# Kernel tuning notes

Measured on AMD Instinct MI355X. Metric: run time of the kernel, lower is better.

## Reference

```python
import jax, jax.numpy as jnp
import numpy as np

D_EMBED, D_K, D_V = 1024, 64, 64
B, S = 4, 4096


def setup_inputs() -> dict:
    key = jax.random.key(0)
    k1, k2, k3, k4 = jax.random.split(key, 4)
    x = jax.random.normal(k1, (B, S, D_EMBED), dtype=jnp.float32)
    # nn.Linear(d_embed, d) stores weight as [d, d_embed]
    Wq = jax.random.normal(k2, (D_K, D_EMBED), dtype=jnp.float32) * (D_EMBED ** -0.5)
    Wk = jax.random.normal(k3, (D_K, D_EMBED), dtype=jnp.float32) * (D_EMBED ** -0.5)
    Wv = jax.random.normal(k4, (D_V, D_EMBED), dtype=jnp.float32) * (D_EMBED ** -0.5)
    return {"x": x, "Wq": Wq, "Wk": Wk, "Wv": Wv}


def reference(x, Wq, Wk, Wv):
    # self-attention: y = z = x
    key = jnp.einsum('bse,ke->bsk', x, Wk)
    query = jnp.einsum('bse,ke->bsk', x, Wq)
    value = jnp.einsum('bse,ve->bsv', x, Wv)
    d_k = key.shape[-1]
    weight = jnp.einsum('bqk,bsk->bqs', query, key) / (d_k ** 0.5)
    # Faithful to torch: tril then masked_fill(weight == 0, -inf)
    weight = jnp.tril(weight)
    weight = jnp.where(weight == 0, -jnp.inf, weight)
    weight = jax.nn.softmax(weight, axis=-1)
    return jnp.einsum('bqs,bsv->bqv', weight, value)
```

## Files before the change

### kernel.cpp

```cpp
#include <hip/hip_runtime.h>
#include <hip/hip_bf16.h>


typedef short s16x8 __attribute__((ext_vector_type(8)));
typedef float f32x4 __attribute__((ext_vector_type(4)));
typedef float f32x16 __attribute__((ext_vector_type(16)));
typedef unsigned u32x2 __attribute__((ext_vector_type(2)));

#define MFMA16(a, b, c) __builtin_amdgcn_mfma_f32_16x16x32_bf16(a, b, c, 0, 0, 0)
#define MFMA32(a, b, c) __builtin_amdgcn_mfma_f32_32x32x16_bf16(a, b, c, 0, 0, 0)

constexpr int SEQ = 4096;
constexpr int DE  = 1024;

__device__ __forceinline__ short f2bf(float f) {
    union { float f; unsigned u; } v; v.f = f;
    unsigned r = (v.u + 0x7FFFu + ((v.u >> 16) & 1u)) >> 16;
    return (short)r;
}
__device__ __forceinline__ unsigned fbits(float f) { union { float f; unsigned u; } v; v.f = f; return v.u; }
__device__ __forceinline__ float bitsf(unsigned u) { union { unsigned u; float f; } v; v.u = u; return v.f; }
__device__ __forceinline__ unsigned pk2(float a, float b) {
    return (fbits(b) & 0xFFFF0000u) | (fbits(a) >> 16);
}

#define GLDS(gp, lp)                                                          \
    __builtin_amdgcn_global_load_lds(                                         \
        (const __attribute__((address_space(1))) unsigned int*)(gp),          \
        (__attribute__((address_space(3))) unsigned int*)(lp), 16, 0, 0)

__global__ __launch_bounds__(256) void k_convw(const float* __restrict__ Wq,
                                               const float* __restrict__ Wk,
                                               const float* __restrict__ Wv,
                                               short* __restrict__ Wb) {
    int i = (blockIdx.x * 256 + threadIdx.x) * 4;
    if (i >= 192 * 1024) return;
    int n = i >> 10, k = i & 1023;
    const float* src; float sc;
    if (n < 64)       { src = Wq + n * 1024;         sc = 0.18033688011112042f; }
    else if (n < 128) { src = Wk + (n - 64) * 1024;  sc = 1.0f; }
    else              { src = Wv + (n - 128) * 1024; sc = 1.0f; }
    float4 v = *(const float4*)(src + k);
    short4 o;
    o.x = f2bf(v.x * sc); o.y = f2bf(v.y * sc);
    o.z = f2bf(v.z * sc); o.w = f2bf(v.w * sc);
    *(short4*)(Wb + i) = o;
}

__global__ __launch_bounds__(512) void k_proj(const float* __restrict__ x,
                                              const short* __restrict__ Wb,
                                              short* __restrict__ Qs,
                                              short* __restrict__ Ks,
                                              short* __restrict__ Vt) {
    __shared__ __align__(16) char lds[2][40960];
    const int tid  = threadIdx.x;
    const int lane = tid & 63;
    const int c = lane & 15, g = (lane >> 4) & 3;
    const int wv = tid >> 6;
    const int rg = wv & 3, nh = wv >> 2;
    const int n0 = nh * 96;
    const int m0 = blockIdx.x * 64;

    const int Ar  = tid >> 4;
    const int Acs = ((tid & 15) << 4) ^ ((Ar & 7) << 4);
    const char* aS0 = (const char*)x + (((size_t)(m0 + Ar)) << 12) + Acs;
    const char* aS1 = aS0 + ((size_t)32 << 12);
    const int Wr  = tid >> 3;
    const int Wcs = ((tid & 7) << 4) ^ ((Wr & 7) << 4);
    const char* wS0 = (const char*)Wb + (((size_t)Wr) << 11) + Wcs;
    const char* wS1 = wS0 + ((size_t)64 << 11);
    const char* wS2 = wS0 + ((size_t)128 << 11);

    char* db0 = &lds[0][0] + tid * 16;
    char* db1 = &lds[1][0] + tid * 16;

    const int arow = rg * 16 + c;
    const int swz  = (c & 7) << 4;
    const char* aR[2] = { &lds[0][0] + arow * 256, &lds[1][0] + arow * 256 };
    const char* wR[2][6];
#pragma unroll
    for (int nf = 0; nf < 6; nf++) {
        int wrow = n0 + nf * 16 + c;
        wR[0][nf] = &lds[0][0] + 16384 + wrow * 128;
        wR[1][nf] = &lds[1][0] + 16384 + wrow * 128;
    }

    f32x4 acc[6];
#pragma unroll
    for (int i = 0; i < 6; i++) acc[i] = (f32x4){0.f, 0.f, 0.f, 0.f};

#define PSTAGE(kk, db) {                                  \
        GLDS(aS0 + (kk) * 256, (db));                     \
        GLDS(aS1 + (kk) * 256, (db) + 8192);              \
        GLDS(wS0 + (kk) * 128, (db) + 16384);             \
        GLDS(wS1 + (kk) * 128, (db) + 24576);             \
        GLDS(wS2 + (kk) * 128, (db) + 32768); }

#define PCOMPUTE(bi) {                                                         \
        _Pragma("unroll")                                                      \
        for (int kc = 0; kc < 2; kc++) {                                       \
            float4 a0 = *(const float4*)(aR[bi] + ((kc*128 + g*32)      ^ swz)); \
            float4 a1 = *(const float4*)(aR[bi] + ((kc*128 + g*32 + 16) ^ swz)); \
            s16x8 a;                                                           \
            a[0]=f2bf(a0.x); a[1]=f2bf(a0.y); a[2]=f2bf(a0.z); a[3]=f2bf(a0.w); \
            a[4]=f2bf(a1.x); a[5]=f2bf(a1.y); a[6]=f2bf(a1.z); a[7]=f2bf(a1.w); \
            _Pragma("unroll")                                                  \
            for (int nf = 0; nf < 6; nf++) {                                   \
                s16x8 bfr = *(const s16x8*)(wR[bi][nf] + ((kc*64 + g*16) ^ swz)); \
                acc[nf] = MFMA16(a, bfr, acc[nf]);                             \
            }                                                                  \
        } }

    PSTAGE(0, db0);
    PSTAGE(1, db1);

    for (int kk = 0; kk < 15; kk++) {
        asm volatile("s_waitcnt vmcnt(5)" ::: "memory");
        __builtin_amdgcn_sched_barrier(0);
        __builtin_amdgcn_s_barrier();
        if (kk & 1) PCOMPUTE(1) else PCOMPUTE(0)
        asm volatile("s_waitcnt lgkmcnt(0)" ::: "memory");
        __builtin_amdgcn_sched_barrier(0);
        __builtin_amdgcn_s_barrier();
        if (kk < 14) { if (kk & 1) PSTAGE(kk + 2, db1) else PSTAGE(kk + 2, db0) }
    }
    asm volatile("s_waitcnt vmcnt(0)" ::: "memory");
    __builtin_amdgcn_sched_barrier(0);
    __builtin_amdgcn_s_barrier();
    PCOMPUTE(1)
#undef PSTAGE
#undef PCOMPUTE

#pragma unroll
    for (int nf = 0; nf < 6; nf++) {
        int col16 = n0 + nf * 16;
        if (col16 < 64) {
            int col = col16 + c;
#pragma unroll
            for (int r = 0; r < 4; r++)
                Qs[(size_t)(m0 + rg * 16 + g * 4 + r) * 64 + col] = f2bf(acc[nf][r]);
        } else if (col16 < 128) {
            int col = col16 - 64 + c;
#pragma unroll
            for (int r = 0; r < 4; r++)
                Ks[(size_t)(m0 + rg * 16 + g * 4 + r) * 64 + col] = f2bf(acc[nf][r]);
        } else {
            int d  = col16 - 128 + c;
            int mm = m0 + rg * 16 + g * 4;
            int bt = mm >> 12, s0 = mm & (SEQ - 1);
            short4 o;
            o.x = f2bf(acc[nf][0]); o.y = f2bf(acc[nf][1]);
            o.z = f2bf(acc[nf][2]); o.w = f2bf(acc[nf][3]);
            *(short4*)(Vt + ((size_t)(bt * 64 + d)) * SEQ + s0) = o;
        }
    }
}

__global__ __launch_bounds__(256) void k_attn(const short* __restrict__ Qs,
                                              const short* __restrict__ Ks,
                                              const short* __restrict__ Vt,
                                              float* __restrict__ out) {
    __shared__ __align__(16) char smem[65536];
    float (*pO)[64][33] = (float (*)[64][33])smem;
    float* pM = (float*)(smem + 33792);
    float* pL = pM + 128;

    int tid = threadIdx.x;
    int l = tid & 63, wv = tid >> 6;
    int q = l & 31, hi = l >> 5;
    int bid = blockIdx.x;
    int j = 127 - (bid >> 2), bt = bid & 3;
    int q0 = j * 32;
    const int kend = q0 + 32;
    const int R = (kend + 127) >> 7;

    const short* Qb = Qs + (size_t)bt * SEQ * 64;
    const short* Kb = Ks + (size_t)bt * SEQ * 64;
    const short* Vb = Vt + (size_t)bt * 64 * SEQ;

    s16x8 qf[4];
#pragma unroll
    for (int d = 0; d < 4; d++)
        qf[d] = *(const s16x8*)(Qb + (size_t)(q0 + q) * 64 + d * 16 + hi * 8);

    const int kr  = l >> 3;
    const int kch = (l & 7) ^ kr;
    const int vr  = l >> 4;

#define ASTAGE(kbase, bufb) {                                                  \
        _Pragma("unroll")                                                      \
        for (int i = 0; i < 4; i++)                                            \
            GLDS(Kb + (((size_t)((kbase) + wv*32 + i*8 + kr)) << 6) + kch*8,   \
                 smem + (bufb)*32768 + (wv*4 + i)*1024);                       \
        _Pragma("unroll")                                                      \
        for (int i = 0; i < 4; i++)                                            \
            GLDS(Vb + (size_t)(wv*16 + i*4 + vr) * SEQ + (kbase)               \
                    + (((l & 15) ^ (i*4 + vr)) * 8),                           \
                 smem + (bufb)*32768 + 16384 + (wv*4 + i)*1024); }

    f32x16 o0 = {}, o1 = {};
    float m = -1e30f, ll = 0.f;

    ASTAGE(0, 0);
    ASTAGE(128, 1);

    for (int r = 0; r < R; r++) {
        if (r == R - 1) asm volatile("s_waitcnt vmcnt(0)" ::: "memory");
        else            asm volatile("s_waitcnt vmcnt(8)" ::: "memory");
        __builtin_amdgcn_sched_barrier(0);
        __builtin_amdgcn_s_barrier();
        __builtin_amdgcn_sched_barrier(0);

        int k0 = r * 128 + wv * 32;
        if (k0 < kend) {
            const char* kb = smem + (r & 1) * 32768 + (wv * 32 + q) * 128;
            int ks = q & 7;
            s16x8 ka0 = *(const s16x8*)(kb + (((hi    ) ^ ks) << 4));
            s16x8 ka1 = *(const s16x8*)(kb + (((hi + 2) ^ ks) << 4));
            s16x8 ka2 = *(const s16x8*)(kb + (((hi + 4) ^ ks) << 4));
            s16x8 ka3 = *(const s16x8*)(kb + (((hi + 6) ^ ks) << 4));
            f32x16 s = {};
            s = MFMA32(ka0, qf[0], s);
            s = MFMA32(ka1, qf[1], s);
            s = MFMA32(ka2, qf[2], s);
            s = MFMA32(ka3, qf[3], s);

            if (k0 + 31 > q0) {
#pragma unroll
                for (int rr = 0; rr < 16; rr++) {
                    int kk = k0 + (rr & 3) + 8 * (rr >> 2) + 4 * hi;
                    if (kk > q0 + q) s[rr] = -3.0e38f;
                }
            }

            float t0 = fmaxf(fmaxf(fmaxf(s[0], s[1]), fmaxf(s[2], s[3])),
                             fmaxf(fmaxf(s[4], s[5]), fmaxf(s[6], s[7])));
            float t1 = fmaxf(fmaxf(fmaxf(s[8], s[9]), fmaxf(s[10], s[11])),
                             fmaxf(fmaxf(s[12], s[13]), fmaxf(s[14], s[15])));
            float tm = fmaxf(t0, t1);
            u32x2 sw = __builtin_amdgcn_permlane32_swap(fbits(tm), fbits(tm), false, false);
            tm = fmaxf(bitsf(sw[0]), bitsf(sw[1]));
            float mn = fmaxf(m, tm);
            float scale = __builtin_amdgcn_exp2f(m - mn);
            m = mn;
#pragma unroll
            for (int rr = 0; rr < 16; rr++) s[rr] = __builtin_amdgcn_exp2f(s[rr] - mn);
            float u0s = ((s[0] + s[1]) + (s[2] + s[3])) + ((s[4] + s[5]) + (s[6] + s[7]));
            float u1s = ((s[8] + s[9]) + (s[10] + s[11])) + ((s[12] + s[13]) + (s[14] + s[15]));
            float ts = u0s + u1s;
            sw = __builtin_amdgcn_permlane32_swap(fbits(ts), fbits(ts), false, false);
            ts = bitsf(sw[0]) + bitsf(sw[1]);
            ll = ll * scale + ts;
            o0 *= scale; o1 *= scale;

            unsigned A0 = pk2(s[0], s[1]),   B0 = pk2(s[2], s[3]);
            unsigned A1 = pk2(s[4], s[5]),   B1 = pk2(s[6], s[7]);
            unsigned A2 = pk2(s[8], s[9]),   B2 = pk2(s[10], s[11]);
            unsigned A3 = pk2(s[12], s[13]), B3 = pk2(s[14], s[15]);
            u32x2 r0 = __builtin_amdgcn_permlane32_swap(A0, A1, false, false);
            u32x2 r1 = __builtin_amdgcn_permlane32_swap(B0, B1, false, false);
            u32x2 r2 = __builtin_amdgcn_permlane32_swap(A2, A3, false, false);
            u32x2 r3 = __builtin_amdgcn_permlane32_swap(B2, B3, false, false);
            union { unsigned u[4]; s16x8 v; } p0u, p1u;
            p0u.u[0] = r0[0]; p0u.u[1] = r1[0]; p0u.u[2] = r0[1]; p0u.u[3] = r1[1];
            p1u.u[0] = r2[0]; p1u.u[1] = r3[0]; p1u.u[2] = r2[1]; p1u.u[3] = r3[1];

            const char* vbb = smem + (r & 1) * 32768 + 16384;
            int vc0 = ((4 * wv + hi)     ^ (q & 15)) << 4;
            int vc1 = ((4 * wv + hi + 2) ^ (q & 15)) << 4;
            const char* v0p = vbb + q * 256;
            const char* v1p = vbb + (q + 32) * 256;
            o0 = MFMA32(*(const s16x8*)(v0p + vc0), p0u.v, o0);
            o0 = MFMA32(*(const s16x8*)(v0p + vc1), p1u.v, o0);
            o1 = MFMA32(*(const s16x8*)(v1p + vc0), p0u.v, o1);
            o1 = MFMA32(*(const s16x8*)(v1p + vc1), p1u.v, o1);
        }

        asm volatile("s_waitcnt lgkmcnt(0)" ::: "memory");
        __builtin_amdgcn_sched_barrier(0);
        __builtin_amdgcn_s_barrier();
        if (r + 2 < R) { if (r & 1) ASTAGE((r + 2) * 128, 1) else ASTAGE((r + 2) * 128, 0) }
    }
#undef ASTAGE

#pragma unroll
    for (int rr = 0; rr < 16; rr++) {
        int dv = (rr & 3) + 8 * (rr >> 2) + 4 * hi;
        pO[wv][dv][q]      = o0[rr];
        pO[wv][dv + 32][q] = o1[rr];
    }
    if (hi == 0) { pM[wv * 32 + q] = m; pL[wv * 32 + q] = ll; }
    __syncthreads();

    int q2 = tid >> 3, d0 = (tid & 7) * 8;
    float m0v = pM[q2], m1v = pM[32 + q2], m2v = pM[64 + q2], m3v = pM[96 + q2];
    float M = fmaxf(fmaxf(m0v, m1v), fmaxf(m2v, m3v));
    float w0 = __builtin_amdgcn_exp2f(m0v - M);
    float w1 = __builtin_amdgcn_exp2f(m1v - M);
    float w2 = __builtin_amdgcn_exp2f(m2v - M);
    float w3 = __builtin_amdgcn_exp2f(m3v - M);
    float L = w0 * pL[q2] + w1 * pL[32 + q2] + w2 * pL[64 + q2] + w3 * pL[96 + q2];
    float inv = 1.0f / L;
    float res[8];
#pragma unroll
    for (int i = 0; i < 8; i++)
        res[i] = (w0 * pO[0][d0 + i][q2] + w1 * pO[1][d0 + i][q2]
                + w2 * pO[2][d0 + i][q2] + w3 * pO[3][d0 + i][q2]) * inv;
    float* op = out + ((size_t)bt * SEQ + q0 + q2) * 64 + d0;
    float4 f0 = {res[0], res[1], res[2], res[3]};
    float4 f1 = {res[4], res[5], res[6], res[7]};
    *(float4*)op = f0;
    *(float4*)(op + 4) = f1;
}

extern "C" void kernel_launch(void* const* d_in, const int* in_sizes, int n_in,
                              void* d_out, int out_size, void* d_ws, size_t ws_size,
                              hipStream_t stream) {
    const float* x  = (const float*)d_in[0];
    const float* Wq = (const float*)d_in[1];
    const float* Wk = (const float*)d_in[2];
    const float* Wv = (const float*)d_in[3];
    float* out = (float*)d_out;

    char* ws = (char*)d_ws;
    short* Wb = (short*)ws;
    short* Qs = (short*)(ws + 393216);
    short* Ks = (short*)(ws + 393216 + 2097152);
    short* Vt = (short*)(ws + 393216 + 2 * 2097152);

    k_convw<<<dim3(192), dim3(256), 0, stream>>>(Wq, Wk, Wv, Wb);
    k_proj <<<dim3(256), dim3(512), 0, stream>>>(x, Wb, Qs, Ks, Vt);
    k_attn <<<dim3(512), dim3(256), 0, stream>>>(Qs, Ks, Vt, out);
}
```

Baseline: 67.37 us.

## Split causal attention KV range into segments with combine kernel; halve projection tile

Measured after the change: 63.10 us. 6.3% less time.

```diff
diff --git a/kernel.cpp b/kernel.cpp
--- a/kernel.cpp
+++ b/kernel.cpp
@@ -47,24 +47,23 @@
     *(short4*)(Wb + i) = o;
 }
 
-__global__ __launch_bounds__(512) void k_proj(const float* __restrict__ x,
-                                              const short* __restrict__ Wb,
-                                              short* __restrict__ Qs,
-                                              short* __restrict__ Ks,
-                                              short* __restrict__ Vt) {
-    __shared__ __align__(16) char lds[2][40960];
+__global__ __launch_bounds__(512, 4) void k_proj(const float* __restrict__ x,
+                                                 const short* __restrict__ Wb,
+                                                 short* __restrict__ Qs,
+                                                 short* __restrict__ Ks,
+                                                 short* __restrict__ Vt) {
+    __shared__ __align__(16) char lds[2][32768];
     const int tid  = threadIdx.x;
     const int lane = tid & 63;
     const int c = lane & 15, g = (lane >> 4) & 3;
     const int wv = tid >> 6;
-    const int rg = wv & 3, nh = wv >> 2;
-    const int n0 = nh * 96;
-    const int m0 = blockIdx.x * 64;
+    const int rg = wv & 1, nh = wv >> 1;
+    const int n0 = nh * 48;
+    const int m0 = blockIdx.x * 32;
 
     const int Ar  = tid >> 4;
     const int Acs = ((tid & 15) << 4) ^ ((Ar & 7) << 4);
     const char* aS0 = (const char*)x + (((size_t)(m0 + Ar)) << 12) + Acs;
-    const char* aS1 = aS0 + ((size_t)32 << 12);
     const int Wr  = tid >> 3;
     const int Wcs = ((tid & 7) << 4) ^ ((Wr & 7) << 4);
     const char* wS0 = (const char*)Wb + (((size_t)Wr) << 11) + Wcs;
@@ -77,24 +76,23 @@
     const int arow = rg * 16 + c;
     const int swz  = (c & 7) << 4;
     const char* aR[2] = { &lds[0][0] + arow * 256, &lds[1][0] + arow * 256 };
-    const char* wR[2][6];
-#pragma unroll
-    for (int nf = 0; nf < 6; nf++) {
+    const char* wR[2][3];
+#pragma unroll
+    for (int nf = 0; nf < 3; nf++) {
         int wrow = n0 + nf * 16 + c;
-        wR[0][nf] = &lds[0][0] + 16384 + wrow * 128;
-        wR[1][nf] = &lds[1][0] + 16384 + wrow * 128;
-    }
-
-    f32x4 acc[6];
-#pragma unroll
-    for (int i = 0; i < 6; i++) acc[i] = (f32x4){0.f, 0.f, 0.f, 0.f};
+        wR[0][nf] = &lds[0][0] + 8192 + wrow * 128;
+        wR[1][nf] = &lds[1][0] + 8192 + wrow * 128;
+    }
+
+    f32x4 acc[3];
+#pragma unroll
+    for (int i = 0; i < 3; i++) acc[i] = (f32x4){0.f, 0.f, 0.f, 0.f};
 
 #define PSTAGE(kk, db) {                                  \
         GLDS(aS0 + (kk) * 256, (db));                     \
-        GLDS(aS1 + (kk) * 256, (db) + 8192);              \
-        GLDS(wS0 + (kk) * 128, (db) + 16384);             \
-        GLDS(wS1 + (kk) * 128, (db) + 24576);             \
-        GLDS(wS2 + (kk) * 128, (db) + 32768); }
+        GLDS(wS0 + (kk) * 128, (db) + 8192);              \
+        GLDS(wS1 + (kk) * 128, (db) + 16384);             \
+        GLDS(wS2 + (kk) * 128, (db) + 24576); }
 
 #define PCOMPUTE(bi) {                                                         \
         _Pragma("unroll")                                                      \
@@ -105,7 +103,7 @@
             a[0]=f2bf(a0.x); a[1]=f2bf(a0.y); a[2]=f2bf(a0.z); a[3]=f2bf(a0.w); \
             a[4]=f2bf(a1.x); a[5]=f2bf(a1.y); a[6]=f2bf(a1.z); a[7]=f2bf(a1.w); \
             _Pragma("unroll")                                                  \
-            for (int nf = 0; nf < 6; nf++) {                                   \
+            for (int nf = 0; nf < 3; nf++) {                                   \
                 s16x8 bfr = *(const s16x8*)(wR[bi][nf] + ((kc*64 + g*16) ^ swz)); \
                 acc[nf] = MFMA16(a, bfr, acc[nf]);                             \
             }                                                                  \
@@ -115,7 +113,7 @@
     PSTAGE(1, db1);
 
     for (int kk = 0; kk < 15; kk++) {
-        asm volatile("s_waitcnt vmcnt(5)" ::: "memory");
+        asm volatile("s_waitcnt vmcnt(4)" ::: "memory");
         __builtin_amdgcn_sched_barrier(0);
         __builtin_amdgcn_s_barrier();
         if (kk & 1) PCOMPUTE(1) else PCOMPUTE(0)
@@ -132,7 +130,7 @@
 #undef PCOMPUTE
 
 #pragma unroll
-    for (int nf = 0; nf < 6; nf++) {
+    for (int nf = 0; nf < 3; nf++) {
         int col16 = n0 + nf * 16;
         if (col16 < 64) {
             int col = col16 + c;
@@ -156,10 +154,10 @@
     }
 }
 
-__global__ __launch_bounds__(256) void k_attn(const short* __restrict__ Qs,
-                                              const short* __restrict__ Ks,
-                                              const short* __restrict__ Vt,
-                                              float* __restrict__ out) {
+__global__ __launch_bounds__(256, 2) void k_attn(const short* __restrict__ Qs,
+                                                 const short* __restrict__ Ks,
+                                                 const short* __restrict__ Vt,
+                                                 float* __restrict__ pws) {
     __shared__ __align__(16) char smem[65536];
     float (*pO)[64][33] = (float (*)[64][33])smem;
     float* pM = (float*)(smem + 33792);
@@ -168,11 +166,18 @@
     int tid = threadIdx.x;
     int l = tid & 63, wv = tid >> 6;
     int q = l & 31, hi = l >> 5;
-    int bid = blockIdx.x;
-    int j = 127 - (bid >> 2), bt = bid & 3;
+
+    int ub = blockIdx.x >> 2, bt = blockIdx.x & 3;
+    int j, seg;
+    if (ub < 128)      { j = 127 - (ub >> 2);       seg = ub & 3; }
+    else if (ub < 224) { int t = ub - 128; j = 95 - t / 3;  seg = t - (t / 3) * 3; }
+    else if (ub < 288) { int t = ub - 224; j = 63 - (t >> 1); seg = t & 1; }
+    else               { j = 31 - (ub - 288);       seg = 0; }
+
     int q0 = j * 32;
-    const int kend = q0 + 32;
-    const int R = (kend + 127) >> 7;
+    int kbase = seg << 10;
+    int kend_u = min(q0 + 32, kbase + 1024);
+    const int R = (kend_u - kbase + 127) >> 7;
 
     const short* Qb = Qs + (size_t)bt * SEQ * 64;
     const short* Kb = Ks + (size_t)bt * SEQ * 64;
@@ -187,22 +192,22 @@
     const int kch = (l & 7) ^ kr;
     const int vr  = l >> 4;
 
-#define ASTAGE(kbase, bufb) {                                                  \
+#define ASTAGE(kb2, bufb) {                                                    \
         _Pragma("unroll")                                                      \
         for (int i = 0; i < 4; i++)                                            \
-            GLDS(Kb + (((size_t)((kbase) + wv*32 + i*8 + kr)) << 6) + kch*8,   \
+            GLDS(Kb + (((size_t)((kb2) + wv*32 + i*8 + kr)) << 6) + kch*8,     \
                  smem + (bufb)*32768 + (wv*4 + i)*1024);                       \
         _Pragma("unroll")                                                      \
         for (int i = 0; i < 4; i++)                                            \
-            GLDS(Vb + (size_t)(wv*16 + i*4 + vr) * SEQ + (kbase)               \
+            GLDS(Vb + (size_t)(wv*16 + i*4 + vr) * SEQ + (kb2)                 \
                     + (((l & 15) ^ (i*4 + vr)) * 8),                           \
                  smem + (bufb)*32768 + 16384 + (wv*4 + i)*1024); }
 
     f32x16 o0 = {}, o1 = {};
     float m = -1e30f, ll = 0.f;
 
-    ASTAGE(0, 0);
-    ASTAGE(128, 1);
+    ASTAGE(kbase, 0);
+    ASTAGE(kbase + 128, 1);
 
     for (int r = 0; r < R; r++) {
         if (r == R - 1) asm volatile("s_waitcnt vmcnt(0)" ::: "memory");
@@ -211,8 +216,8 @@
         __builtin_amdgcn_s_barrier();
         __builtin_amdgcn_sched_barrier(0);
 
-        int k0 = r * 128 + wv * 32;
-        if (k0 < kend) {
+        int k0 = kbase + r * 128 + wv * 32;
+        if (k0 < kend_u) {
             const char* kb = smem + (r & 1) * 32768 + (wv * 32 + q) * 128;
             int ks = q & 7;
             s16x8 ka0 = *(const s16x8*)(kb + (((hi    ) ^ ks) << 4));
@@ -279,7 +284,7 @@
         asm volatile("s_waitcnt lgkmcnt(0)" ::: "memory");
         __builtin_amdgcn_sched_barrier(0);
         __builtin_amdgcn_s_barrier();
-        if (r + 2 < R) { if (r & 1) ASTAGE((r + 2) * 128, 1) else ASTAGE((r + 2) * 128, 0) }
+        if (r + 2 < R) { if (r & 1) ASTAGE(kbase + (r + 2) * 128, 1) else ASTAGE(kbase + (r + 2) * 128, 0) }
     }
 #undef ASTAGE
 
@@ -300,15 +305,51 @@
     float w2 = __builtin_amdgcn_exp2f(m2v - M);
     float w3 = __builtin_amdgcn_exp2f(m3v - M);
     float L = w0 * pL[q2] + w1 * pL[32 + q2] + w2 * pL[64 + q2] + w3 * pL[96 + q2];
+    float res[8];
+#pragma unroll
+    for (int i = 0; i < 8; i++)
+        res[i] = w0 * pO[0][d0 + i][q2] + w1 * pO[1][d0 + i][q2]
+               + w2 * pO[2][d0 + i][q2] + w3 * pO[3][d0 + i][q2];
+    float* p = pws + (size_t)(((bt << 7) + j) * 4 + seg) * 2112;
+    float4 f0 = {res[0], res[1], res[2], res[3]};
+    float4 f1 = {res[4], res[5], res[6], res[7]};
+    *(float4*)(p + q2 * 64 + d0) = f0;
+    *(float4*)(p + q2 * 64 + d0 + 4) = f1;
+    if ((tid & 7) == 0) { p[2048 + q2] = M; p[2080 + q2] = L; }
+}
+
+__global__ __launch_bounds__(256) void k_comb(const float* __restrict__ pws,
+                                              float* __restrict__ out) {
+    int bid = blockIdx.x;
+    int bt = bid >> 7, j = bid & 127;
+    int nseg = (j >> 5) + 1;
+    int tid = threadIdx.x;
+    int q2 = tid >> 3, d0 = (tid & 7) * 8;
+    const float* base = pws + (size_t)(bid * 4) * 2112;
+
+    float ms[4], wsg[4];
+    float M = -1e30f;
+#pragma unroll 4
+    for (int s = 0; s < nseg; s++) { ms[s] = base[s * 2112 + 2048 + q2]; M = fmaxf(M, ms[s]); }
+    float L = 0.f;
+#pragma unroll 4
+    for (int s = 0; s < nseg; s++) {
+        wsg[s] = __builtin_amdgcn_exp2f(ms[s] - M);
+        L += wsg[s] * base[s * 2112 + 2080 + q2];
+    }
     float inv = 1.0f / L;
     float res[8];
 #pragma unroll
-    for (int i = 0; i < 8; i++)
-        res[i] = (w0 * pO[0][d0 + i][q2] + w1 * pO[1][d0 + i][q2]
-                + w2 * pO[2][d0 + i][q2] + w3 * pO[3][d0 + i][q2]) * inv;
-    float* op = out + ((size_t)bt * SEQ + q0 + q2) * 64 + d0;
-    float4 f0 = {res[0], res[1], res[2], res[3]};
-    float4 f1 = {res[4], res[5], res[6], res[7]};
+    for (int i = 0; i < 8; i++) res[i] = 0.f;
+#pragma unroll 4
+    for (int s = 0; s < nseg; s++) {
+        const float* po = base + s * 2112 + q2 * 64 + d0;
+#pragma unroll
+        for (int i = 0; i < 8; i++) res[i] += wsg[s] * po[i];
+    }
+    float* op = out + ((size_t)bt * SEQ + j * 32 + q2) * 64 + d0;
+    float4 f0 = {res[0] * inv, res[1] * inv, res[2] * inv, res[3] * inv};
+    float4 f1 = {res[4] * inv, res[5] * inv, res[6] * inv, res[7] * inv};
     *(float4*)op = f0;
     *(float4*)(op + 4) = f1;
 }
@@ -327,8 +368,10 @@
     short* Qs = (short*)(ws + 393216);
     short* Ks = (short*)(ws + 393216 + 2097152);
     short* Vt = (short*)(ws + 393216 + 2 * 2097152);
-
-    k_convw<<<dim3(192), dim3(256), 0, stream>>>(Wq, Wk, Wv, Wb);
-    k_proj <<<dim3(256), dim3(512), 0, stream>>>(x, Wb, Qs, Ks, Vt);
-    k_attn <<<dim3(512), dim3(256), 0, stream>>>(Qs, Ks, Vt, out);
-}
+    float* pP = (float*)(ws + 6684672);
+
+    k_convw<<<dim3(192),  dim3(256), 0, stream>>>(Wq, Wk, Wv, Wb);
+    k_proj <<<dim3(512),  dim3(512), 0, stream>>>(x, Wb, Qs, Ks, Vt);
+    k_attn <<<dim3(1280), dim3(256), 0, stream>>>(Qs, Ks, Vt, pP);
+    k_comb <<<dim3(512),  dim3(256), 0, stream>>>(pP, out);
+}
```

## Split causal attention into KV segments with separate combine kernel

Applied to the files above, without the earlier changes.

Result: no change. 67.56 us (+0.3%).

```diff
diff --git a/kernel.cpp b/kernel.cpp
--- a/kernel.cpp
+++ b/kernel.cpp
@@ -156,23 +156,25 @@
     }
 }
 
-__global__ __launch_bounds__(256) void k_attn(const short* __restrict__ Qs,
-                                              const short* __restrict__ Ks,
-                                              const short* __restrict__ Vt,
-                                              float* __restrict__ out) {
-    __shared__ __align__(16) char smem[65536];
-    float (*pO)[64][33] = (float (*)[64][33])smem;
-    float* pM = (float*)(smem + 33792);
-    float* pL = pM + 128;
+__global__ __launch_bounds__(256, 3) void k_attn(const short* __restrict__ Qs,
+                                                 const short* __restrict__ Ks,
+                                                 const short* __restrict__ Vt,
+                                                 float* __restrict__ pws) {
+    __shared__ __align__(16) char smem[2][16384];
 
     int tid = threadIdx.x;
     int l = tid & 63, wv = tid >> 6;
     int q = l & 31, hi = l >> 5;
-    int bid = blockIdx.x;
-    int j = 127 - (bid >> 2), bt = bid & 3;
-    int q0 = j * 32;
-    const int kend = q0 + 32;
-    const int R = (kend + 127) >> 7;
+
+    int ub = blockIdx.x >> 2, bt = blockIdx.x & 3;
+    int u = ub, j = 31, cs = 8;
+    while (u >= cs) { u -= cs; --j; cs = (j + 4) >> 2; }
+    int seg = u;
+    int kb0 = seg << 9;
+    int kend_t = min(j * 128 + 128, kb0 + 512);
+    const int R = (kend_t - kb0 + 63) >> 6;
+    int q0 = j * 128 + wv * 32;
+    int mycend = q0 + 32;
 
     const short* Qb = Qs + (size_t)bt * SEQ * 64;
     const short* Kb = Ks + (size_t)bt * SEQ * 64;
@@ -183,132 +185,182 @@
     for (int d = 0; d < 4; d++)
         qf[d] = *(const s16x8*)(Qb + (size_t)(q0 + q) * 64 + d * 16 + hi * 8);
 
-    const int kr  = l >> 3;
-    const int kch = (l & 7) ^ kr;
-    const int vr  = l >> 4;
-
-#define ASTAGE(kbase, bufb) {                                                  \
+    const int row8 = l >> 3;
+    const int scs  = (l & 7) ^ row8;
+
+#define ASTAGE(kb, b) {                                                        \
         _Pragma("unroll")                                                      \
-        for (int i = 0; i < 4; i++)                                            \
-            GLDS(Kb + (((size_t)((kbase) + wv*32 + i*8 + kr)) << 6) + kch*8,   \
-                 smem + (bufb)*32768 + (wv*4 + i)*1024);                       \
-        _Pragma("unroll")                                                      \
-        for (int i = 0; i < 4; i++)                                            \
-            GLDS(Vb + (size_t)(wv*16 + i*4 + vr) * SEQ + (kbase)               \
-                    + (((l & 15) ^ (i*4 + vr)) * 8),                           \
-                 smem + (bufb)*32768 + 16384 + (wv*4 + i)*1024); }
+        for (int i = 0; i < 2; i++) {                                          \
+            GLDS(Kb + (((size_t)((kb) + wv*16 + i*8 + row8)) << 6) + scs*8,    \
+                 &smem[b][0] + (wv*16 + i*8)*128);                             \
+            GLDS(Vb + (size_t)(wv*16 + i*8 + row8) * SEQ + (kb) + scs*8,       \
+                 &smem[b][0] + 8192 + (wv*16 + i*8)*128); } }
 
     f32x16 o0 = {}, o1 = {};
     float m = -1e30f, ll = 0.f;
-
-    ASTAGE(0, 0);
-    ASTAGE(128, 1);
+    const int qs7 = q & 7;
+
+    ASTAGE(kb0, 0);
+    if (R > 1) ASTAGE(kb0 + 64, 1);
 
     for (int r = 0; r < R; r++) {
         if (r == R - 1) asm volatile("s_waitcnt vmcnt(0)" ::: "memory");
-        else            asm volatile("s_waitcnt vmcnt(8)" ::: "memory");
+        else            asm volatile("s_waitcnt vmcnt(4)" ::: "memory");
         __builtin_amdgcn_sched_barrier(0);
         __builtin_amdgcn_s_barrier();
         __builtin_amdgcn_sched_barrier(0);
 
-        int k0 = r * 128 + wv * 32;
-        if (k0 < kend) {
-            const char* kb = smem + (r & 1) * 32768 + (wv * 32 + q) * 128;
-            int ks = q & 7;
-            s16x8 ka0 = *(const s16x8*)(kb + (((hi    ) ^ ks) << 4));
-            s16x8 ka1 = *(const s16x8*)(kb + (((hi + 2) ^ ks) << 4));
-            s16x8 ka2 = *(const s16x8*)(kb + (((hi + 4) ^ ks) << 4));
-            s16x8 ka3 = *(const s16x8*)(kb + (((hi + 6) ^ ks) << 4));
-            f32x16 s = {};
-            s = MFMA32(ka0, qf[0], s);
-            s = MFMA32(ka1, qf[1], s);
-            s = MFMA32(ka2, qf[2], s);
-            s = MFMA32(ka3, qf[3], s);
-
+        int k0 = kb0 + r * 64;
+        if (k0 < mycend) {
+            const char* kl = &smem[r & 1][0];
+            f32x16 sa = {}, sb = {};
+#pragma unroll
+            for (int dd = 0; dd < 4; dd++) {
+                int ch = ((2 * dd + hi) ^ qs7) << 4;
+                s16x8 ka = *(const s16x8*)(kl + q * 128 + ch);
+                s16x8 kb2 = *(const s16x8*)(kl + (32 + q) * 128 + ch);
+                sa = MFMA32(ka,  qf[dd], sa);
+                sb = MFMA32(kb2, qf[dd], sb);
+            }
             if (k0 + 31 > q0) {
 #pragma unroll
                 for (int rr = 0; rr < 16; rr++) {
-                    int kk = k0 + (rr & 3) + 8 * (rr >> 2) + 4 * hi;
-                    if (kk > q0 + q) s[rr] = -3.0e38f;
+                    int kv = k0 + (rr & 3) + 8 * (rr >> 2) + 4 * hi;
+                    if (kv > q0 + q) sa[rr] = -3.0e38f;
                 }
             }
-
-            float t0 = fmaxf(fmaxf(fmaxf(s[0], s[1]), fmaxf(s[2], s[3])),
-                             fmaxf(fmaxf(s[4], s[5]), fmaxf(s[6], s[7])));
-            float t1 = fmaxf(fmaxf(fmaxf(s[8], s[9]), fmaxf(s[10], s[11])),
-                             fmaxf(fmaxf(s[12], s[13]), fmaxf(s[14], s[15])));
+            if (k0 + 63 > q0) {
+#pragma unroll
+                for (int rr = 0; rr < 16; rr++) {
+                    int kv = k0 + 32 + (rr & 3) + 8 * (rr >> 2) + 4 * hi;
+                    if (kv > q0 + q) sb[rr] = -3.0e38f;
+                }
+            }
+            float t0 = -3.0e38f, t1 = -3.0e38f;
+#pragma unroll
+            for (int rr = 0; rr < 16; rr++) { t0 = fmaxf(t0, sa[rr]); t1 = fmaxf(t1, sb[rr]); }
             float tm = fmaxf(t0, t1);
             u32x2 sw = __builtin_amdgcn_permlane32_swap(fbits(tm), fbits(tm), false, false);
             tm = fmaxf(bitsf(sw[0]), bitsf(sw[1]));
             float mn = fmaxf(m, tm);
             float scale = __builtin_amdgcn_exp2f(m - mn);
             m = mn;
-#pragma unroll
-            for (int rr = 0; rr < 16; rr++) s[rr] = __builtin_amdgcn_exp2f(s[rr] - mn);
-            float u0s = ((s[0] + s[1]) + (s[2] + s[3])) + ((s[4] + s[5]) + (s[6] + s[7]));
-            float u1s = ((s[8] + s[9]) + (s[10] + s[11])) + ((s[12] + s[13]) + (s[14] + s[15]));
-            float ts = u0s + u1s;
-            sw = __builtin_amdgcn_permlane32_swap(fbits(ts), fbits(ts), false, false);
-            ts = bitsf(sw[0]) + bitsf(sw[1]);
-            ll = ll * scale + ts;
+            float ss = 0.f;
+#pragma unroll
+            for (int rr = 0; rr < 16; rr++) {
+                sa[rr] = __builtin_amdgcn_exp2f(sa[rr] - mn);
+                sb[rr] = __builtin_amdgcn_exp2f(sb[rr] - mn);
+                ss += sa[rr] + sb[rr];
+            }
+            sw = __builtin_amdgcn_permlane32_swap(fbits(ss), fbits(ss), false, false);
+            ss = bitsf(sw[0]) + bitsf(sw[1]);
+            ll = ll * scale + ss;
             o0 *= scale; o1 *= scale;
 
-            unsigned A0 = pk2(s[0], s[1]),   B0 = pk2(s[2], s[3]);
-            unsigned A1 = pk2(s[4], s[5]),   B1 = pk2(s[6], s[7]);
-            unsigned A2 = pk2(s[8], s[9]),   B2 = pk2(s[10], s[11]);
-            unsigned A3 = pk2(s[12], s[13]), B3 = pk2(s[14], s[15]);
-            u32x2 r0 = __builtin_amdgcn_permlane32_swap(A0, A1, false, false);
-            u32x2 r1 = __builtin_amdgcn_permlane32_swap(B0, B1, false, false);
-            u32x2 r2 = __builtin_amdgcn_permlane32_swap(A2, A3, false, false);
-            u32x2 r3 = __builtin_amdgcn_permlane32_swap(B2, B3, false, false);
-            union { unsigned u[4]; s16x8 v; } p0u, p1u;
-            p0u.u[0] = r0[0]; p0u.u[1] = r1[0]; p0u.u[2] = r0[1]; p0u.u[3] = r1[1];
-            p1u.u[0] = r2[0]; p1u.u[1] = r3[0]; p1u.u[2] = r2[1]; p1u.u[3] = r3[1];
-
-            const char* vbb = smem + (r & 1) * 32768 + 16384;
-            int vc0 = ((4 * wv + hi)     ^ (q & 15)) << 4;
-            int vc1 = ((4 * wv + hi + 2) ^ (q & 15)) << 4;
-            const char* v0p = vbb + q * 256;
-            const char* v1p = vbb + (q + 32) * 256;
-            o0 = MFMA32(*(const s16x8*)(v0p + vc0), p0u.v, o0);
-            o0 = MFMA32(*(const s16x8*)(v0p + vc1), p1u.v, o0);
-            o1 = MFMA32(*(const s16x8*)(v1p + vc0), p0u.v, o1);
-            o1 = MFMA32(*(const s16x8*)(v1p + vc1), p1u.v, o1);
+            union { unsigned u[4]; s16x8 v; } pA0, pA1, pB0, pB1;
+            {
+                unsigned A0 = pk2(sa[0], sa[1]),   B0 = pk2(sa[2], sa[3]);
+                unsigned A1 = pk2(sa[4], sa[5]),   B1 = pk2(sa[6], sa[7]);
+                unsigned A2 = pk2(sa[8], sa[9]),   B2 = pk2(sa[10], sa[11]);
+                unsigned A3 = pk2(sa[12], sa[13]), B3 = pk2(sa[14], sa[15]);
+                u32x2 r0 = __builtin_amdgcn_permlane32_swap(A0, A1, false, false);
+                u32x2 r1 = __builtin_amdgcn_permlane32_swap(B0, B1, false, false);
+                u32x2 r2 = __builtin_amdgcn_permlane32_swap(A2, A3, false, false);
+                u32x2 r3 = __builtin_amdgcn_permlane32_swap(B2, B3, false, false);
+                pA0.u[0] = r0[0]; pA0.u[1] = r1[0]; pA0.u[2] = r0[1]; pA0.u[3] = r1[1];
+                pA1.u[0] = r2[0]; pA1.u[1] = r3[0]; pA1.u[2] = r2[1]; pA1.u[3] = r3[1];
+            }
+            {
+                unsigned A0 = pk2(sb[0], sb[1]),   B0 = pk2(sb[2], sb[3]);
+                unsigned A1 = pk2(sb[4], sb[5]),   B1 = pk2(sb[6], sb[7]);
+                unsigned A2 = pk2(sb[8], sb[9]),   B2 = pk2(sb[10], sb[11]);
+                unsigned A3 = pk2(sb[12], sb[13]), B3 = pk2(sb[14], sb[15]);
+                u32x2 r0 = __builtin_amdgcn_permlane32_swap(A0, A1, false, false);
+                u32x2 r1 = __builtin_amdgcn_permlane32_swap(B0, B1, false, false);
+                u32x2 r2 = __builtin_amdgcn_permlane32_swap(A2, A3, false, false);
+                u32x2 r3 = __builtin_amdgcn_permlane32_swap(B2, B3, false, false);
+                pB0.u[0] = r0[0]; pB0.u[1] = r1[0]; pB0.u[2] = r0[1]; pB0.u[3] = r1[1];
+                pB1.u[0] = r2[0]; pB1.u[1] = r3[0]; pB1.u[2] = r2[1]; pB1.u[3] = r3[1];
+            }
+
+            const char* vl = &smem[r & 1][0] + 8192;
+            const char* v0p = vl + q * 128;
+            const char* v1p = vl + (32 + q) * 128;
+            int c0 = ((0 + hi) ^ qs7) << 4, c1 = ((2 + hi) ^ qs7) << 4;
+            int c2 = ((4 + hi) ^ qs7) << 4, c3 = ((6 + hi) ^ qs7) << 4;
+            o0 = MFMA32(*(const s16x8*)(v0p + c0), pA0.v, o0);
+            o0 = MFMA32(*(const s16x8*)(v0p + c1), pA1.v, o0);
+            o0 = MFMA32(*(const s16x8*)(v0p + c2), pB0.v, o0);
+            o0 = MFMA32(*(const s16x8*)(v0p + c3), pB1.v, o0);
+            o1 = MFMA32(*(const s16x8*)(v1p + c0), pA0.v, o1);
+            o1 = MFMA32(*(const s16x8*)(v1p + c1), pA1.v, o1);
+            o1 = MFMA32(*(const s16x8*)(v1p + c2), pB0.v, o1);
+            o1 = MFMA32(*(const s16x8*)(v1p + c3), pB1.v, o1);
         }
 
         asm volatile("s_waitcnt lgkmcnt(0)" ::: "memory");
         __builtin_amdgcn_sched_barrier(0);
         __builtin_amdgcn_s_barrier();
-        if (r + 2 < R) { if (r & 1) ASTAGE((r + 2) * 128, 1) else ASTAGE((r + 2) * 128, 0) }
+        if (r + 2 < R) { if (r & 1) ASTAGE(kb0 + (r + 2) * 64, 1) else ASTAGE(kb0 + (r + 2) * 64, 0) }
     }
 #undef ASTAGE
 
+    float* p = pws + ((size_t)blockIdx.x * 4 + wv) * 2112;
 #pragma unroll
     for (int rr = 0; rr < 16; rr++) {
         int dv = (rr & 3) + 8 * (rr >> 2) + 4 * hi;
-        pO[wv][dv][q]      = o0[rr];
-        pO[wv][dv + 32][q] = o1[rr];
-    }
-    if (hi == 0) { pM[wv * 32 + q] = m; pL[wv * 32 + q] = ll; }
-    __syncthreads();
-
-    int q2 = tid >> 3, d0 = (tid & 7) * 8;
-    float m0v = pM[q2], m1v = pM[32 + q2], m2v = pM[64 + q2], m3v = pM[96 + q2];
-    float M = fmaxf(fmaxf(m0v, m1v), fmaxf(m2v, m3v));
-    float w0 = __builtin_amdgcn_exp2f(m0v - M);
-    float w1 = __builtin_amdgcn_exp2f(m1v - M);
-    float w2 = __builtin_amdgcn_exp2f(m2v - M);
-    float w3 = __builtin_amdgcn_exp2f(m3v - M);
-    float L = w0 * pL[q2] + w1 * pL[32 + q2] + w2 * pL[64 + q2] + w3 * pL[96 + q2];
+        p[dv * 32 + q]        = o0[rr];
+        p[(dv + 32) * 32 + q] = o1[rr];
+    }
+    if (hi == 0) { p[2048 + q] = m; p[2080 + q] = ll; }
+}
+
+__global__ __launch_bounds__(256) void k_comb(const float* __restrict__ pws,
+                                              float* __restrict__ out) {
+    int b = blockIdx.x;
+    int bt = b & 3, j = (b >> 2) & 31, w = b >> 7;
+    int nseg = (j + 4) >> 2;
+    int ubb = 0;
+    for (int jj = 31; jj > j; --jj) ubb += (jj + 4) >> 2;
+
+    int tid = threadIdx.x;
+    int q = tid >> 3, dv0 = (tid & 7) * 8;
+
+    const float* rec[8];
+    float ms[8];
+    float M = -1e30f;
+#pragma unroll
+    for (int s = 0; s < 8; s++) {
+        if (s < nseg) {
+            rec[s] = pws + ((size_t)(((ubb + s) * 4 + bt) * 4 + w)) * 2112;
+            ms[s] = rec[s][2048 + q];
+            M = fmaxf(M, ms[s]);
+        }
+    }
+    float L = 0.f, wsg[8];
+#pragma unroll
+    for (int s = 0; s < 8; s++) {
+        if (s < nseg) {
+            wsg[s] = __builtin_amdgcn_exp2f(ms[s] - M);
+            L += wsg[s] * rec[s][2080 + q];
+        }
+    }
     float inv = 1.0f / L;
     float res[8];
 #pragma unroll
-    for (int i = 0; i < 8; i++)
-        res[i] = (w0 * pO[0][d0 + i][q2] + w1 * pO[1][d0 + i][q2]
-                + w2 * pO[2][d0 + i][q2] + w3 * pO[3][d0 + i][q2]) * inv;
-    float* op = out + ((size_t)bt * SEQ + q0 + q2) * 64 + d0;
-    float4 f0 = {res[0], res[1], res[2], res[3]};
-    float4 f1 = {res[4], res[5], res[6], res[7]};
+    for (int i = 0; i < 8; i++) res[i] = 0.f;
+#pragma unroll
+    for (int s = 0; s < 8; s++) {
+        if (s < nseg) {
+#pragma unroll
+            for (int i = 0; i < 8; i++)
+                res[i] += wsg[s] * rec[s][(dv0 + i) * 32 + q];
+        }
+    }
+    int qout = j * 128 + w * 32 + q;
+    float* op = out + ((size_t)bt * SEQ + qout) * 64 + dv0;
+    float4 f0 = {res[0] * inv, res[1] * inv, res[2] * inv, res[3] * inv};
+    float4 f1 = {res[4] * inv, res[5] * inv, res[6] * inv, res[7] * inv};
     *(float4*)op = f0;
     *(float4*)(op + 4) = f1;
 }
@@ -327,8 +379,10 @@
     short* Qs = (short*)(ws + 393216);
     short* Ks = (short*)(ws + 393216 + 2097152);
     short* Vt = (short*)(ws + 393216 + 2 * 2097152);
+    float* pP = (float*)(ws + 6684672);
 
     k_convw<<<dim3(192), dim3(256), 0, stream>>>(Wq, Wk, Wv, Wb);
     k_proj <<<dim3(256), dim3(512), 0, stream>>>(x, Wb, Qs, Ks, Vt);
-    k_attn <<<dim3(512), dim3(256), 0, stream>>>(Qs, Ks, Vt, out);
-}
+    k_attn <<<dim3(576), dim3(256), 0, stream>>>(Qs, Ks, Vt, pP);
+    k_comb <<<dim3(512), dim3(256), 0, stream>>>(pP, out);
+}
```
